# Kernel tuning notes

Hardware: AMD Instinct MI355X
Metric: run time of the kernel (lower is better)

The kernel has to match this reference:

```python
import jax, jax.numpy as jnp
import numpy as np

B, S, D_IN, D_OUT = 4, 2048, 1024, 1024

def setup_inputs() -> dict:
    key = jax.random.key(0)
    k0, k1, k2, k3 = jax.random.split(key, 4)
    sc = 1.0 / np.sqrt(D_IN)
    return {
        "x": jax.random.normal(k0, (B, S, D_IN), dtype=jnp.float32),
        "wq": jax.random.normal(k1, (D_OUT, D_IN), dtype=jnp.float32) * sc,
        "wk": jax.random.normal(k2, (D_OUT, D_IN), dtype=jnp.float32) * sc,
        "wv": jax.random.normal(k3, (D_OUT, D_IN), dtype=jnp.float32) * sc,
    }

def reference(x, wq, wk, wv):
    # Linear (no bias): y = x @ W.T, W shaped [d_out, d_in]
    q = jnp.einsum("bsd,ed->bse", x, wq)
    k = jnp.einsum("bsd,ed->bse", x, wk)
    v = jnp.einsum("bsd,ed->bse", x, wv)
    scores = jnp.einsum("bqe,bke->bqk", q, k)  # [B,S,S]
    n = x.shape[1]
    causal = jnp.triu(jnp.ones((n, n), dtype=bool), k=1)  # True above diagonal -> masked
    scores = jnp.where(causal, -jnp.inf, scores)
    attn = jax.nn.softmax(scores / jnp.sqrt(jnp.asarray(k.shape[-1], scores.dtype)), axis=-1)
    # dropout p=0.0 -> identity
    return jnp.einsum("bqk,bke->bqe", attn, v)
```

## Files before the change

kernel.cpp:

```cpp
#include <hip/hip_runtime.h>

#define Bb 4
#define Ss 2048
#define Dd 1024

typedef unsigned short u16;
typedef __bf16 bf16x8 __attribute__((ext_vector_type(8)));
typedef float  f32x4  __attribute__((ext_vector_type(4)));

__device__ inline u16 f2bf(float f) {
  union { float f; unsigned u; } x; x.f = f;
  unsigned u = x.u;
  return (u16)((u + 0x7fffu + ((u >> 16) & 1u)) >> 16);
}
__device__ inline float bf2f(u16 h) {
  union { unsigned u; float f; } x; x.u = ((unsigned)h) << 16;
  return x.f;
}

__device__ static inline void gl_lds16(const u16* g, u16* l) {
  __builtin_amdgcn_global_load_lds((__attribute__((address_space(1))) const void*)g,
                                   (__attribute__((address_space(3))) void*)l,
                                   16, 0, 0);
}

__global__ __launch_bounds__(256) void cast_all(const float* __restrict__ x,
                                                const float* __restrict__ wq,
                                                const float* __restrict__ wk,
                                                const float* __restrict__ wv,
                                                u16* __restrict__ xb,
                                                u16* __restrict__ wb,
                                                float* __restrict__ lsum) {
  int id = blockIdx.x;
  if (id < 8) {
    float4 z = {0.f, 0.f, 0.f, 0.f};
    ((float4*)lsum)[id * 256 + threadIdx.x] = z;
  }
  const float* src; u16* dst; int off;
  if (id < 2048) {
    src = x; dst = xb; off = id * 4096;
  } else {
    int wi = id - 2048;
    int w = wi >> 8;
    src = (w == 0) ? wq : (w == 1) ? wk : wv;
    dst = wb + (size_t)w * Dd * Dd;
    off = (wi & 255) * 4096;
  }
#pragma unroll
  for (int t = 0; t < 4; t++) {
    int i = off + t * 1024 + threadIdx.x * 4;
    float4 v = *(const float4*)(src + i);
    unsigned p0 = (unsigned)f2bf(v.x) | ((unsigned)f2bf(v.y) << 16);
    unsigned p1 = (unsigned)f2bf(v.z) | ((unsigned)f2bf(v.w) << 16);
    uint2 p; p.x = p0; p.y = p1;
    *(uint2*)(dst + i) = p;
  }
}

#define BM 128
#define BN 128

__device__ inline void gemm_tile(const u16* __restrict__ A, int lda,
                                 const u16* __restrict__ Bp, int ldb,
                                 int kBeg, int kEnd,
                                 u16* lds, f32x4 acc[4][4]) {
  u16* lA0 = lds;
  u16* lB0 = lds + 4096;
  u16* lA1 = lds + 8192;
  u16* lB1 = lds + 12288;
  const int tid  = threadIdx.x;
  const int lane = tid & 63, wave = tid >> 6;
  const int quad = lane >> 4, r16 = lane & 15;
  const int wm = (wave & 1) * 64, wn = (wave >> 1) * 64;
  const int r0 = tid >> 2, part = tid & 3;

  for (int k0 = kBeg; k0 < kEnd; k0 += 64) {
    __syncthreads();
#pragma unroll
    for (int q = 0; q < 2; q++) {
      int row = q * 64 + r0;
      int s8 = (q * 256 + tid) * 8;
      const u16* ga = A  + (size_t)row * lda + k0 + part * 8;
      const u16* gb = Bp + (size_t)row * ldb + k0 + part * 8;
      gl_lds16(ga,      lA0 + s8);
      gl_lds16(gb,      lB0 + s8);
      gl_lds16(ga + 32, lA1 + s8);
      gl_lds16(gb + 32, lB1 + s8);
    }
    __syncthreads();
#pragma unroll
    for (int h = 0; h < 2; h++) {
      const u16* la = h ? lA1 : lA0;
      const u16* lb = h ? lB1 : lB0;
      bf16x8 fa[4], fb[4];
#pragma unroll
      for (int t = 0; t < 4; t++)
        fa[t] = *(const bf16x8*)(la + (wm + t * 16 + r16) * 32 + quad * 8);
#pragma unroll
      for (int t = 0; t < 4; t++)
        fb[t] = *(const bf16x8*)(lb + (wn + t * 16 + r16) * 32 + quad * 8);
#pragma unroll
      for (int tm = 0; tm < 4; tm++)
#pragma unroll
        for (int tn = 0; tn < 4; tn++)
          acc[tm][tn] = __builtin_amdgcn_mfma_f32_16x16x32_bf16(fa[tm], fb[tn],
                                                                acc[tm][tn], 0, 0, 0);
    }
  }
}

__global__ __launch_bounds__(256) void qkv_gemm(const u16* __restrict__ xb,
                                                const u16* __restrict__ wb,
                                                u16* __restrict__ qkv) {
  __shared__ __align__(16) u16 shmem[16384];
  const int id  = blockIdx.x;
  const int xcd = id & 7, j = id >> 3;
  const int xt  = j & 7;
  const int yl  = (j >> 3) & 7;
  const int zi  = j >> 6;
  const int y   = xcd * 8 + yl;
  const int row0 = y * BM;
  const int col0 = xt * BN;
  const u16* A  = xb + (size_t)row0 * Dd;
  const u16* Bp = wb + (size_t)zi * Dd * Dd + (size_t)col0 * Dd;
  f32x4 acc[4][4];
  const f32x4 zero = {0.f, 0.f, 0.f, 0.f};
#pragma unroll
  for (int tm = 0; tm < 4; tm++)
#pragma unroll
    for (int tn = 0; tn < 4; tn++) acc[tm][tn] = zero;

  gemm_tile(A, Dd, Bp, Dd, 0, Dd, shmem, acc);

  u16* out = qkv + (size_t)zi * ((size_t)Bb * Ss * Dd);
  const int lane = threadIdx.x & 63, wave = threadIdx.x >> 6;
  const int quad = lane >> 4, r16 = lane & 15;
  const int wm = (wave & 1) * 64, wn = (wave >> 1) * 64;
#pragma unroll
  for (int tm = 0; tm < 4; tm++)
#pragma unroll
    for (int tn = 0; tn < 4; tn++) {
      int rr = row0 + wm + tm * 16 + quad * 4;
      int cc = col0 + wn + tn * 16 + r16;
#pragma unroll
      for (int r = 0; r < 4; r++)
        out[(size_t)(rr + r) * Dd + cc] = f2bf(acc[tm][tn][r]);
    }
}

__global__ __launch_bounds__(256) void scores_fused(const u16* __restrict__ qb,
                                                    const u16* __restrict__ kb,
                                                    const u16* __restrict__ vb,
                                                    u16* __restrict__ sc,
                                                    u16* __restrict__ vt,
                                                    float* __restrict__ lsum) {
  __shared__ __align__(16) u16 shmem[16384];
  const int id = blockIdx.x;
  const int tid = threadIdx.x;

  if (id >= 544) {
    const int bid = id - 544;
    u16 (*t)[72] = (u16(*)[72])shmem;
    for (int u = bid; u < 2048; u += 480) {
      const int b = u >> 9, rem = u & 511;
      const int e0 = (rem >> 5) * 64, s0 = (rem & 31) * 64;
      const u16* src = vb + (size_t)b * Ss * Dd;
      u16* dst = vt + (size_t)b * Dd * Ss;
      if (u != bid) __syncthreads();
#pragma unroll
      for (int gg = tid; gg < 512; gg += 256) {
        int row = gg >> 3, prt = gg & 7;
        uint4 v = *(const uint4*)(src + (size_t)(s0 + row) * Dd + e0 + prt * 8);
        const u16* pv = (const u16*)&v;
#pragma unroll
        for (int jj = 0; jj < 8; jj++) t[prt * 8 + jj][row] = pv[jj];
      }
      __syncthreads();
#pragma unroll
      for (int gg = tid; gg < 512; gg += 256) {
        int ee = gg >> 3, prt = gg & 7;
        uint4 v = *(const uint4*)(&t[ee][prt * 8]);
        *(uint4*)(dst + (size_t)(e0 + ee) * Ss + s0 + prt * 8) = v;
      }
    }
    return;
  }

  const int xcd = id & 7, j = id >> 3;
  const int b = j / 17, tloc = j - b * 17;
  const int t = xcd * 17 + tloc;
  int it = (int)((sqrtf(8.f * (float)t + 1.f) - 1.f) * 0.5f);
  while ((it + 1) * (it + 2) / 2 <= t) it++;
  while (it * (it + 1) / 2 > t) it--;
  const int jt = t - it * (it + 1) / 2;

  const u16* A  = qb + (size_t)b * Ss * Dd + (size_t)it * BM * Dd;
  const u16* Bp = kb + (size_t)b * Ss * Dd + (size_t)jt * BN * Dd;
  f32x4 acc[4][4];
  const f32x4 zero = {0.f, 0.f, 0.f, 0.f};
#pragma unroll
  for (int tm = 0; tm < 4; tm++)
#pragma unroll
    for (int tn = 0; tn < 4; tn++) acc[tm][tn] = zero;

  gemm_tile(A, Dd, Bp, Dd, 0, Dd, shmem, acc);

  u16* out = sc + (size_t)b * Ss * Ss;
  float* lr = lsum + (size_t)b * Ss;
  const int lane = tid & 63, wave = tid >> 6;
  const int quad = lane >> 4, r16 = lane & 15;
  const int wm = (wave & 1) * 64, wn = (wave >> 1) * 64;
#pragma unroll
  for (int tm = 0; tm < 4; tm++) {
    float psum[4] = {0.f, 0.f, 0.f, 0.f};
#pragma unroll
    for (int tn = 0; tn < 4; tn++) {
      int rr = it * BM + wm + tm * 16 + quad * 4;
      int cc = jt * BN + wn + tn * 16 + r16;
#pragma unroll
      for (int r = 0; r < 4; r++) {
        float p = 0.f;
        u16 h = 0;
        if (cc <= rr + r) {
          h = f2bf(__expf(acc[tm][tn][r] * 0.03125f));
          p = bf2f(h);
        }
        out[(size_t)(rr + r) * Ss + cc] = h;
        psum[r] += p;
      }
    }
#pragma unroll
    for (int r = 0; r < 4; r++) {
      float s = psum[r];
      s += __shfl_xor(s, 1);
      s += __shfl_xor(s, 2);
      s += __shfl_xor(s, 4);
      s += __shfl_xor(s, 8);
      if (r16 == 0) {
        int row = it * BM + wm + tm * 16 + quad * 4 + r;
        atomicAdd(&lr[row], s);
      }
    }
  }
}

__global__ __launch_bounds__(256) void pv_gemm(const u16* __restrict__ sc,
                                               const u16* __restrict__ vt,
                                               const float* __restrict__ lsum,
                                               float* __restrict__ out) {
  __shared__ __align__(16) u16 shmem[16384];
  const int idx = blockIdx.x;
  const int slot = idx >> 5;
  const int it = (slot < 8) ? (15 - 2 * slot) : (2 * (slot - 8));
  const int rem = idx & 31;
  const int col0 = (rem & 7) * BN;
  const int b = rem >> 3;
  const int row0 = it * BM;
  const u16* A  = sc + (size_t)b * Ss * Ss + (size_t)row0 * Ss;
  const u16* Bp = vt + (size_t)b * Dd * Ss + (size_t)col0 * Ss;
  f32x4 acc[4][4];
  const f32x4 zero = {0.f, 0.f, 0.f, 0.f};
#pragma unroll
  for (int tm = 0; tm < 4; tm++)
#pragma unroll
    for (int tn = 0; tn < 4; tn++) acc[tm][tn] = zero;

  gemm_tile(A, Ss, Bp, Ss, 0, row0 + BM, shmem, acc);

  float* o = out + (size_t)b * Ss * Dd;
  const float* lr = lsum + (size_t)b * Ss;
  const int lane = threadIdx.x & 63, wave = threadIdx.x >> 6;
  const int quad = lane >> 4, r16 = lane & 15;
  const int wm = (wave & 1) * 64, wn = (wave >> 1) * 64;
#pragma unroll
  for (int tm = 0; tm < 4; tm++) {
    int rbase = row0 + wm + tm * 16 + quad * 4;
    float s0 = 1.f / lr[rbase], s1 = 1.f / lr[rbase + 1];
    float s2 = 1.f / lr[rbase + 2], s3 = 1.f / lr[rbase + 3];
#pragma unroll
    for (int tn = 0; tn < 4; tn++) {
      int cc = col0 + wn + tn * 16 + r16;
      o[(size_t)(rbase + 0) * Dd + cc] = acc[tm][tn][0] * s0;
      o[(size_t)(rbase + 1) * Dd + cc] = acc[tm][tn][1] * s1;
      o[(size_t)(rbase + 2) * Dd + cc] = acc[tm][tn][2] * s2;
      o[(size_t)(rbase + 3) * Dd + cc] = acc[tm][tn][3] * s3;
    }
  }
}

extern "C" void kernel_launch(void* const* d_in, const int* in_sizes, int n_in,
                              void* d_out, int out_size, void* d_ws, size_t ws_size,
                              hipStream_t stream) {
  const float* x  = (const float*)d_in[0];
  const float* wq = (const float*)d_in[1];
  const float* wk = (const float*)d_in[2];
  const float* wv = (const float*)d_in[3];
  float* out = (float*)d_out;
  char* ws = (char*)d_ws;
  if (ws_size < 106987520u) return;

  u16* qkv  = (u16*)(ws);
  u16* sc   = (u16*)(ws + 50331648u);
  u16* xb   = (u16*)(ws + 83886080u);
  u16* vt   = xb;
  u16* wb   = (u16*)(ws + 100663296u);
  float* lsum = (float*)(ws + 106954752u);

  const size_t nQ = (size_t)Bb * Ss * Dd;

  cast_all<<<2816, 256, 0, stream>>>(x, wq, wk, wv, xb, wb, lsum);
  qkv_gemm<<<1536, 256, 0, stream>>>(xb, wb, qkv);
  scores_fused<<<1024, 256, 0, stream>>>(qkv, qkv + nQ, qkv + 2 * nQ, sc, vt, lsum);
  pv_gemm<<<512, 256, 0, stream>>>(sc, vt, lsum, out);
}
```

Measured before the change: 237.3 us.

## Fuse V transpose into QKV GEMM epilogue and reorder PV tile schedule

The V projection blocks now write their output already transposed through an LDS staging buffer directly into the vt layout. This removes the separate transpose blocks that ran inside the scores kernel, along with the extra round trip of V through global memory. The scores kernel shrinks to 544 blocks, and the PV GEMM block-to-tile mapping is reordered to interleave heavy and light causal row tiles. Costs are two extra barriers in the V epilogue and a different scheduling balance in the PV kernel.

```diff
diff --git a/kernel.cpp b/kernel.cpp
--- a/kernel.cpp
+++ b/kernel.cpp
@@ -111,7 +111,8 @@
 
 __global__ __launch_bounds__(256) void qkv_gemm(const u16* __restrict__ xb,
                                                 const u16* __restrict__ wb,
-                                                u16* __restrict__ qkv) {
+                                                u16* __restrict__ qk,
+                                                u16* __restrict__ vt) {
   __shared__ __align__(16) u16 shmem[16384];
   const int id  = blockIdx.x;
   const int xcd = id & 7, j = id >> 3;
@@ -132,60 +133,60 @@
 
   gemm_tile(A, Dd, Bp, Dd, 0, Dd, shmem, acc);
 
-  u16* out = qkv + (size_t)zi * ((size_t)Bb * Ss * Dd);
-  const int lane = threadIdx.x & 63, wave = threadIdx.x >> 6;
+  const int tid = threadIdx.x;
+  const int lane = tid & 63, wave = tid >> 6;
   const int quad = lane >> 4, r16 = lane & 15;
   const int wm = (wave & 1) * 64, wn = (wave >> 1) * 64;
-#pragma unroll
-  for (int tm = 0; tm < 4; tm++)
-#pragma unroll
-    for (int tn = 0; tn < 4; tn++) {
-      int rr = row0 + wm + tm * 16 + quad * 4;
-      int cc = col0 + wn + tn * 16 + r16;
-#pragma unroll
-      for (int r = 0; r < 4; r++)
-        out[(size_t)(rr + r) * Dd + cc] = f2bf(acc[tm][tn][r]);
-    }
-}
-
-__global__ __launch_bounds__(256) void scores_fused(const u16* __restrict__ qb,
-                                                    const u16* __restrict__ kb,
-                                                    const u16* __restrict__ vb,
-                                                    u16* __restrict__ sc,
-                                                    u16* __restrict__ vt,
-                                                    float* __restrict__ lsum) {
+
+  if (zi < 2) {
+    u16* out = qk + (size_t)zi * ((size_t)Bb * Ss * Dd);
+#pragma unroll
+    for (int tm = 0; tm < 4; tm++)
+#pragma unroll
+      for (int tn = 0; tn < 4; tn++) {
+        int rr = row0 + wm + tm * 16 + quad * 4;
+        int cc = col0 + wn + tn * 16 + r16;
+#pragma unroll
+        for (int r = 0; r < 4; r++)
+          out[(size_t)(rr + r) * Dd + cc] = f2bf(acc[tm][tn][r]);
+      }
+    return;
+  }
+
+  const int b = row0 >> 11, srow = row0 & 2047;
+  u16* vtb = vt + (size_t)b * Dd * Ss;
+#pragma unroll
+  for (int p = 0; p < 2; p++) {
+    __syncthreads();
+    if ((wave >> 1) == p) {
+#pragma unroll
+      for (int tm = 0; tm < 4; tm++)
+#pragma unroll
+        for (int tn = 0; tn < 4; tn++) {
+          int cl = tn * 16 + r16;
+          int rr4 = wm + tm * 16 + quad * 4;
+          u16 pk[4];
+#pragma unroll
+          for (int r = 0; r < 4; r++) pk[r] = f2bf(acc[tm][tn][r]);
+          *(uint2*)(shmem + cl * 136 + rr4) = *(const uint2*)pk;
+        }
+    }
+    __syncthreads();
+    const u16* lr_ = shmem + (tid >> 2) * 136 + (tid & 3) * 32;
+    u16* gp = vtb + (size_t)(col0 + p * 64 + (tid >> 2)) * Ss + srow + (tid & 3) * 32;
+#pragma unroll
+    for (int jj = 0; jj < 4; jj++)
+      *(uint4*)(gp + jj * 8) = *(const uint4*)(lr_ + jj * 8);
+  }
+}
+
+__global__ __launch_bounds__(256) void scores_kernel(const u16* __restrict__ qb,
+                                                     const u16* __restrict__ kb,
+                                                     u16* __restrict__ sc,
+                                                     float* __restrict__ lsum) {
   __shared__ __align__(16) u16 shmem[16384];
   const int id = blockIdx.x;
   const int tid = threadIdx.x;
-
-  if (id >= 544) {
-    const int bid = id - 544;
-    u16 (*t)[72] = (u16(*)[72])shmem;
-    for (int u = bid; u < 2048; u += 480) {
-      const int b = u >> 9, rem = u & 511;
-      const int e0 = (rem >> 5) * 64, s0 = (rem & 31) * 64;
-      const u16* src = vb + (size_t)b * Ss * Dd;
-      u16* dst = vt + (size_t)b * Dd * Ss;
-      if (u != bid) __syncthreads();
-#pragma unroll
-      for (int gg = tid; gg < 512; gg += 256) {
-        int row = gg >> 3, prt = gg & 7;
-        uint4 v = *(const uint4*)(src + (size_t)(s0 + row) * Dd + e0 + prt * 8);
-        const u16* pv = (const u16*)&v;
-#pragma unroll
-        for (int jj = 0; jj < 8; jj++) t[prt * 8 + jj][row] = pv[jj];
-      }
-      __syncthreads();
-#pragma unroll
-      for (int gg = tid; gg < 512; gg += 256) {
-        int ee = gg >> 3, prt = gg & 7;
-        uint4 v = *(const uint4*)(&t[ee][prt * 8]);
-        *(uint4*)(dst + (size_t)(e0 + ee) * Ss + s0 + prt * 8) = v;
-      }
-    }
-    return;
-  }
-
   const int xcd = id & 7, j = id >> 3;
   const int b = j / 17, tloc = j - b * 17;
   const int t = xcd * 17 + tloc;
@@ -250,11 +251,12 @@
                                                float* __restrict__ out) {
   __shared__ __align__(16) u16 shmem[16384];
   const int idx = blockIdx.x;
-  const int slot = idx >> 5;
-  const int it = (slot < 8) ? (15 - 2 * slot) : (2 * (slot - 8));
-  const int rem = idx & 31;
-  const int col0 = (rem & 7) * BN;
-  const int b = rem >> 3;
+  const int sp = idx & 7;
+  const int bc = (idx >> 3) & 31;
+  const int half = idx >> 8;
+  const int it = half ? sp : (15 - sp);
+  const int b = bc >> 3;
+  const int col0 = (bc & 7) * BN;
   const int row0 = it * BM;
   const u16* A  = sc + (size_t)b * Ss * Ss + (size_t)row0 * Ss;
   const u16* Bp = vt + (size_t)b * Dd * Ss + (size_t)col0 * Ss;
@@ -299,17 +301,17 @@
   char* ws = (char*)d_ws;
   if (ws_size < 106987520u) return;
 
-  u16* qkv  = (u16*)(ws);
+  u16* qk   = (u16*)(ws);
+  u16* vt   = (u16*)(ws + 33554432u);
   u16* sc   = (u16*)(ws + 50331648u);
   u16* xb   = (u16*)(ws + 83886080u);
-  u16* vt   = xb;
   u16* wb   = (u16*)(ws + 100663296u);
   float* lsum = (float*)(ws + 106954752u);
 
   const size_t nQ = (size_t)Bb * Ss * Dd;
 
   cast_all<<<2816, 256, 0, stream>>>(x, wq, wk, wv, xb, wb, lsum);
-  qkv_gemm<<<1536, 256, 0, stream>>>(xb, wb, qkv);
-  scores_fused<<<1024, 256, 0, stream>>>(qkv, qkv + nQ, qkv + 2 * nQ, sc, vt, lsum);
+  qkv_gemm<<<1536, 256, 0, stream>>>(xb, wb, qk, vt);
+  scores_kernel<<<544, 256, 0, stream>>>(qk, qk + nQ, sc, lsum);
   pv_gemm<<<512, 256, 0, stream>>>(sc, vt, lsum, out);
 }
```

After: 243.2 us. +2.5%, slower.
